# Kernel optimization log

Hardware: AMD Instinct MI355X
Metric: run time of the kernel (lower is better)

Reference implementation:

```python
import jax, jax.numpy as jnp
import numpy as np

B, S, D, H = 8, 1024, 1024, 16
HD = D // H  # head dim = 64


def setup_inputs() -> dict:
    key = jax.random.key(0)
    ks = jax.random.split(key, 8)
    return {
        "hidden_states": jax.random.normal(ks[0], (B, S, D), dtype=jnp.float32),
        "attention_mask": jnp.zeros((B, 1, 1, S), dtype=jnp.float32),
        "Wq": jax.random.normal(ks[1], (D, D), dtype=jnp.float32) * (1.0 / np.sqrt(D)),
        "bq": jax.random.normal(ks[2], (D,), dtype=jnp.float32) * 0.02,
        "Wk": jax.random.normal(ks[3], (D, D), dtype=jnp.float32) * (1.0 / np.sqrt(D)),
        "bk": jax.random.normal(ks[4], (D,), dtype=jnp.float32) * 0.02,
        "Wv": jax.random.normal(ks[5], (D, D), dtype=jnp.float32) * (1.0 / np.sqrt(D)),
        "bv": jax.random.normal(ks[6], (D,), dtype=jnp.float32) * 0.02,
    }


def _split_heads(x):
    # [B,S,D] -> [B,H,S,HD]
    return x.reshape(B, S, H, HD).transpose(0, 2, 1, 3)


def reference(hidden_states, attention_mask, Wq, bq, Wk, bk, Wv, bv):
    q = _split_heads(hidden_states @ Wq + bq)
    k = _split_heads(hidden_states @ Wk + bk)
    v = _split_heads(hidden_states @ Wv + bv)
    # [B,H,S,S]
    scores = jnp.einsum("bhqd,bhkd->bhqk", q, k) / jnp.sqrt(jnp.float32(HD))
    scores = scores + attention_mask
    probs = jax.nn.softmax(scores, axis=-1)  # dropout p=0.0 (eval)
    ctx = jnp.einsum("bhqk,bhkd->bhqd", probs, v)
    # [B,H,S,HD] -> [B,S,D]
    return ctx.transpose(0, 2, 1, 3).reshape(B, S, D)
```

## Files before the change

kernel.cpp:

```cpp
#include <hip/hip_runtime.h>
#include <stdint.h>

#define BB 8
#define SS 1024
#define DD 1024
#define HH 16
#define HDIM 64

typedef __bf16 bf16x8 __attribute__((ext_vector_type(8)));
typedef float f32x4 __attribute__((ext_vector_type(4)));

__device__ __forceinline__ unsigned short f2bf(float f) {
    union { float f; unsigned u; } v; v.f = f;
    unsigned r = v.u + 0x7fff + ((v.u >> 16) & 1);
    return (unsigned short)(r >> 16);
}

__device__ __forceinline__ float exp2fast(float x) {
#if __has_builtin(__builtin_amdgcn_exp2f)
    return __builtin_amdgcn_exp2f(x);
#else
    return __expf(x * 0.69314718f);
#endif
}

__device__ __forceinline__ void async16(void* lds, const void* g) {
    __builtin_amdgcn_global_load_lds(
        (const __attribute__((address_space(1))) unsigned int*)g,
        (__attribute__((address_space(3))) unsigned int*)lds, 16, 0, 0);
}

__global__ __launch_bounds__(256) void convert_x(const float* __restrict__ x,
                                                 unsigned short* __restrict__ xb, int n) {
    int i = (blockIdx.x * 256 + threadIdx.x) * 4;
    if (i < n) {
        float4 f = *reinterpret_cast<const float4*>(x + i);
        ushort4 o;
        o.x = f2bf(f.x); o.y = f2bf(f.y); o.z = f2bf(f.z); o.w = f2bf(f.w);
        *reinterpret_cast<ushort4*>(xb + i) = o;
    }
}

__global__ __launch_bounds__(256) void transpose_w(const float* __restrict__ w0,
                                                   const float* __restrict__ w1,
                                                   const float* __restrict__ w2,
                                                   unsigned short* __restrict__ t0,
                                                   unsigned short* __restrict__ t1,
                                                   unsigned short* __restrict__ t2) {
    const float* w = (blockIdx.z == 0) ? w0 : (blockIdx.z == 1) ? w1 : w2;
    unsigned short* wt = (blockIdx.z == 0) ? t0 : (blockIdx.z == 1) ? t1 : t2;
    __shared__ unsigned short tile[64][65];
    int k0 = blockIdx.x * 64, n0 = blockIdx.y * 64;
    #pragma unroll
    for (int i = 0; i < 16; ++i) {
        int idx = threadIdx.x + i * 256;
        int r = idx >> 6, c = idx & 63;
        tile[r][c] = f2bf(w[(k0 + r) * DD + n0 + c]);
    }
    __syncthreads();
    #pragma unroll
    for (int i = 0; i < 16; ++i) {
        int idx = threadIdx.x + i * 256;
        int r = idx >> 6, c = idx & 63;
        wt[(n0 + r) * DD + k0 + c] = tile[c][r];
    }
}

__global__ __launch_bounds__(256) void gemm_qkv(
    const unsigned short* __restrict__ xb,
    const unsigned short* __restrict__ wt0, const unsigned short* __restrict__ wt1,
    const unsigned short* __restrict__ wt2,
    const float* __restrict__ b0, const float* __restrict__ b1, const float* __restrict__ b2,
    unsigned short* __restrict__ qo, unsigned short* __restrict__ ko,
    unsigned short* __restrict__ vto)
{
    const unsigned short* wt; const float* bias; unsigned short* out;
    if (blockIdx.z == 0)      { wt = wt0; bias = b0; out = qo; }
    else if (blockIdx.z == 1) { wt = wt1; bias = b1; out = ko; }
    else                      { wt = wt2; bias = b2; out = vto; }

    __shared__ unsigned short As[2][128 * 32];
    __shared__ unsigned short Bs[2][128 * 32];

    int m0 = blockIdx.x * 128, n0 = blockIdx.y * 128;
    int tid = threadIdx.x;
    int wave = tid >> 6, lane = tid & 63, lq = lane >> 4, lm = lane & 15;
    int wr = wave >> 1, wc = wave & 1;

    f32x4 acc[4][4] = {};

    int row0 = tid >> 2, s = tid & 3;
    int c0 = (s - (row0 >> 1)) & 3;
    const unsigned short* ga0 = xb + (m0 + row0) * DD + c0 * 8;
    const unsigned short* ga1 = ga0 + 64 * DD;
    const unsigned short* gb0 = wt + (n0 + row0) * DD + c0 * 8;
    const unsigned short* gb1 = gb0 + 64 * DD;

    int slot = ((lq + (lm >> 1)) & 3) * 8;

    async16(&As[0][tid * 8], ga0);  async16(&As[0][(tid + 256) * 8], ga1);
    async16(&Bs[0][tid * 8], gb0);  async16(&Bs[0][(tid + 256) * 8], gb1);
    ga0 += 32; ga1 += 32; gb0 += 32; gb1 += 32;

    for (int t = 0; t < 32; ++t) {
        int p = t & 1;
        __syncthreads();
        if (t < 31) {
            async16(&As[p ^ 1][tid * 8], ga0);  async16(&As[p ^ 1][(tid + 256) * 8], ga1);
            async16(&Bs[p ^ 1][tid * 8], gb0);  async16(&Bs[p ^ 1][(tid + 256) * 8], gb1);
            ga0 += 32; ga1 += 32; gb0 += 32; gb1 += 32;
        }
        bf16x8 a[4], b[4];
        #pragma unroll
        for (int i = 0; i < 4; ++i)
            a[i] = *reinterpret_cast<const bf16x8*>(&As[p][(wr * 64 + i * 16 + lm) * 32 + slot]);
        #pragma unroll
        for (int j = 0; j < 4; ++j)
            b[j] = *reinterpret_cast<const bf16x8*>(&Bs[p][(wc * 64 + j * 16 + lm) * 32 + slot]);
        #pragma unroll
        for (int i = 0; i < 4; ++i)
            #pragma unroll
            for (int j = 0; j < 4; ++j)
                acc[i][j] = __builtin_amdgcn_mfma_f32_16x16x32_bf16(a[i], b[j], acc[i][j], 0, 0, 0);
    }

    if (blockIdx.z == 2) {
        #pragma unroll
        for (int j = 0; j < 4; ++j) {
            int col = n0 + wc * 64 + j * 16 + lm;
            float bsv = bias[col];
            int h = col >> 6, hd = col & 63;
            #pragma unroll
            for (int i = 0; i < 4; ++i) {
                int m = m0 + wr * 64 + i * 16 + lq * 4;
                int b_ = m >> 10, sr = m & 1023;
                ushort4 pk;
                pk.x = f2bf(acc[i][j][0] + bsv);
                pk.y = f2bf(acc[i][j][1] + bsv);
                pk.z = f2bf(acc[i][j][2] + bsv);
                pk.w = f2bf(acc[i][j][3] + bsv);
                *reinterpret_cast<ushort4*>(out + (((b_ * HH + h) * HDIM + hd) << 10) + sr) = pk;
            }
        }
    } else {
        #pragma unroll
        for (int j = 0; j < 4; ++j) {
            int col = n0 + wc * 64 + j * 16 + lm;
            float bsv = bias[col];
            int h = col >> 6, hd = col & 63;
            #pragma unroll
            for (int i = 0; i < 4; ++i) {
                #pragma unroll
                for (int r = 0; r < 4; ++r) {
                    int m = m0 + wr * 64 + i * 16 + lq * 4 + r;
                    int b_ = m >> 10, sr = m & 1023;
                    out[(((b_ * HH + h) << 10) + sr) * HDIM + hd] = f2bf(acc[i][j][r] + bsv);
                }
            }
        }
    }
}

__global__ __launch_bounds__(256) void attention(
    const unsigned short* __restrict__ q,
    const unsigned short* __restrict__ k,
    const unsigned short* __restrict__ vt,
    const float* __restrict__ mask,
    float* __restrict__ out)
{
    __shared__ unsigned short Ks[2][64 * 64];
    __shared__ unsigned short Vs[2][64 * 64];
    __shared__ unsigned short Ps[4][16 * 72];
    __shared__ float msk[SS];

    int blk = blockIdx.x;
    int xcd = blk & 7, j = blk >> 3;
    int bh = (xcd << 4) + (j >> 4);
    int qt = j & 15;
    int b = bh >> 4, h = bh & 15;

    int tid = threadIdx.x;
    int wave = tid >> 6, lane = tid & 63, lq = lane >> 4, lm = lane & 15;

    const unsigned short* qp = q + (size_t)bh * SS * HDIM;
    const unsigned short* kp = k + (size_t)bh * SS * HDIM;
    const unsigned short* vp = vt + (size_t)bh * HDIM * SS;

    for (int i = tid; i < SS; i += 256) msk[i] = mask[b * SS + i] * 1.44269504f;

    int qrow = qt * 64 + wave * 16 + lm;
    bf16x8 qa0 = *reinterpret_cast<const bf16x8*>(qp + qrow * HDIM + lq * 8);
    bf16x8 qa1 = *reinterpret_cast<const bf16x8*>(qp + qrow * HDIM + 32 + lq * 8);

    float lsum = 0.f;
    f32x4 o[4] = {};

    int row0 = tid >> 3, sg = tid & 7;
    int cg = (sg - row0) & 7;
    const unsigned short* gk = kp + row0 * 64 + cg * 8;
    const unsigned short* gv = vp + row0 * SS + cg * 8;

    int sl0 = ((lq + lm) & 7) * 8;
    int sl1 = ((lq + lm + 4) & 7) * 8;

    async16(&Ks[0][tid * 8], gk);  async16(&Ks[0][(tid + 256) * 8], gk + 32 * 64);
    async16(&Vs[0][tid * 8], gv);  async16(&Vs[0][(tid + 256) * 8], gv + 32 * SS);
    gk += 64 * 64; gv += 64;

    unsigned short* Pw = Ps[wave];

    for (int t = 0; t < 16; ++t) {
        int p = t & 1;
        __syncthreads();
        if (t < 15) {
            async16(&Ks[p ^ 1][tid * 8], gk);  async16(&Ks[p ^ 1][(tid + 256) * 8], gk + 32 * 64);
            async16(&Vs[p ^ 1][tid * 8], gv);  async16(&Vs[p ^ 1][(tid + 256) * 8], gv + 32 * SS);
            gk += 64 * 64; gv += 64;
        }
        int kb0 = t * 64;

        f32x4 c[4];
        #pragma unroll
        for (int nb = 0; nb < 4; ++nb) {
            bf16x8 kf0 = *reinterpret_cast<const bf16x8*>(&Ks[p][(nb * 16 + lm) * 64 + sl0]);
            bf16x8 kf1 = *reinterpret_cast<const bf16x8*>(&Ks[p][(nb * 16 + lm) * 64 + sl1]);
            f32x4 z = {};
            z = __builtin_amdgcn_mfma_f32_16x16x32_bf16(kf0, qa0, z, 0, 0, 0);
            z = __builtin_amdgcn_mfma_f32_16x16x32_bf16(kf1, qa1, z, 0, 0, 0);
            c[nb] = z;
        }

        #pragma unroll
        for (int nb = 0; nb < 4; ++nb) {
            float4 mk = *reinterpret_cast<const float4*>(&msk[kb0 + nb * 16 + lq * 4]);
            unsigned u[4];
            #pragma unroll
            for (int r = 0; r < 4; ++r) {
                float e = exp2fast(fmaf(c[nb][r], 0.18033688f,
                                        reinterpret_cast<const float*>(&mk)[r]));
                union { float f; unsigned v; } cv; cv.f = e;
                u[r] = cv.v;
                union { unsigned v; float f; } tr; tr.v = cv.v & 0xffff0000u;
                lsum += tr.f;
            }
            uint2 pk;
            pk.x = __builtin_amdgcn_perm(u[1], u[0], 0x07060302u);
            pk.y = __builtin_amdgcn_perm(u[3], u[2], 0x07060302u);
            *reinterpret_cast<uint2*>(&Pw[lm * 72 + nb * 16 + lq * 4]) = pk;
        }

        #pragma unroll
        for (int ks = 0; ks < 2; ++ks) {
            bf16x8 pa = *reinterpret_cast<const bf16x8*>(&Pw[lm * 72 + ks * 32 + lq * 8]);
            int slv = (ks == 0) ? sl0 : sl1;
            #pragma unroll
            for (int nb2 = 0; nb2 < 4; ++nb2) {
                bf16x8 vf = *reinterpret_cast<const bf16x8*>(&Vs[p][(nb2 * 16 + lm) * 64 + slv]);
                o[nb2] = __builtin_amdgcn_mfma_f32_16x16x32_bf16(pa, vf, o[nb2], 0, 0, 0);
            }
        }
    }

    lsum += __shfl_xor(lsum, 16, 64);
    lsum += __shfl_xor(lsum, 32, 64);
    float linv[4];
    #pragma unroll
    for (int r = 0; r < 4; ++r)
        linv[r] = 1.0f / __shfl(lsum, lq * 4 + r, 64);

    #pragma unroll
    for (int nb2 = 0; nb2 < 4; ++nb2) {
        #pragma unroll
        for (int r = 0; r < 4; ++r) {
            int sr = qt * 64 + wave * 16 + lq * 4 + r;
            out[((size_t)(b * SS + sr)) * DD + h * HDIM + nb2 * 16 + lm] = o[nb2][r] * linv[r];
        }
    }
}

extern "C" void kernel_launch(void* const* d_in, const int* in_sizes, int n_in,
                              void* d_out, int out_size, void* d_ws, size_t ws_size,
                              hipStream_t stream) {
    const float* hs   = (const float*)d_in[0];
    const float* mask = (const float*)d_in[1];
    const float* Wq   = (const float*)d_in[2];
    const float* bq   = (const float*)d_in[3];
    const float* Wk   = (const float*)d_in[4];
    const float* bk   = (const float*)d_in[5];
    const float* Wv   = (const float*)d_in[6];
    const float* bv   = (const float*)d_in[7];
    float* out = (float*)d_out;

    char* ws = (char*)d_ws;
    unsigned short* Xb  = (unsigned short*)(ws);
    unsigned short* WT0 = (unsigned short*)(ws + 16777216);
    unsigned short* WT1 = (unsigned short*)(ws + 18874368);
    unsigned short* WT2 = (unsigned short*)(ws + 20971520);
    unsigned short* qw  = (unsigned short*)(ws + 23068672);
    unsigned short* kw  = (unsigned short*)(ws + 39845888);
    unsigned short* vtw = (unsigned short*)(ws + 56623104);

    convert_x<<<8192, 256, 0, stream>>>(hs, Xb, BB * SS * DD);
    transpose_w<<<dim3(16, 16, 3), 256, 0, stream>>>(Wq, Wk, Wv, WT0, WT1, WT2);
    gemm_qkv<<<dim3(64, 8, 3), 256, 0, stream>>>(Xb, WT0, WT1, WT2,
                                                 bq, bk, bv, qw, kw, vtw);
    attention<<<2048, 256, 0, stream>>>(qw, kw, vtw, mask, out);
}
```

Before: 249.3 us.

## Pre-pack QKV operands into MFMA fragment layout and load directly from global

Merges the x conversion and weight transpose into one prep kernel that writes bf16 data already arranged in MFMA fragment order. The QKV GEMM then reads fragments straight from global memory into registers with software double-buffering, dropping the LDS staging and the barriers that went with it. It also adds XCD-aware block remapping for L2 reuse and stages Q/K output through LDS so stores are coalesced. The bf16 rounding in the epilogue becomes a cheaper round-half-up with a perm instruction. The risk is lower reuse, because every wave now fetches its own operands from L2 instead of sharing one LDS tile across the block.

```diff
diff --git a/kernel.cpp b/kernel.cpp
--- a/kernel.cpp
+++ b/kernel.cpp
@@ -30,133 +30,177 @@
         (__attribute__((address_space(3))) unsigned int*)lds, 16, 0, 0);
 }
 
-__global__ __launch_bounds__(256) void convert_x(const float* __restrict__ x,
-                                                 unsigned short* __restrict__ xb, int n) {
-    int i = (blockIdx.x * 256 + threadIdx.x) * 4;
-    if (i < n) {
-        float4 f = *reinterpret_cast<const float4*>(x + i);
+__global__ __launch_bounds__(256) void prep(
+    const float* __restrict__ x, unsigned short* __restrict__ xf,
+    const float* __restrict__ w0, const float* __restrict__ w1,
+    const float* __restrict__ w2,
+    unsigned short* __restrict__ f0, unsigned short* __restrict__ f1,
+    unsigned short* __restrict__ f2)
+{
+    __shared__ unsigned short tile[64 * 76];
+    int bid = blockIdx.x;
+    int tid = threadIdx.x;
+    if (bid < 2048) {
+        int mt = bid >> 4, kt = bid & 15;
+        const float* src = x + (size_t)(mt * 64) * DD + kt * 64;
+        #pragma unroll
+        for (int i = 0; i < 4; ++i) {
+            int f = tid + i * 256;
+            int r = f >> 4, c4 = f & 15;
+            float4 v = *reinterpret_cast<const float4*>(src + r * DD + c4 * 4);
+            ushort4 o;
+            o.x = f2bf(v.x); o.y = f2bf(v.y); o.z = f2bf(v.z); o.w = f2bf(v.w);
+            *reinterpret_cast<ushort4*>(&tile[r * 76 + c4 * 4]) = o;
+        }
+        __syncthreads();
+        #pragma unroll
+        for (int i = 0; i < 2; ++i) {
+            int s = tid + i * 256;
+            int frag = s >> 6, l = s & 63;
+            int m_l = (frag & 3) * 16 + (l & 15);
+            int k_l = (frag >> 2) * 32 + ((l >> 4) & 3) * 8;
+            uint4 v = *reinterpret_cast<const uint4*>(&tile[m_l * 76 + k_l]);
+            int fm = mt * 4 + (frag & 3);
+            int fk = kt * 2 + (frag >> 2);
+            *reinterpret_cast<uint4*>(xf + (size_t)((fm * 32 + fk) * 64 + l) * 8) = v;
+        }
+        return;
+    }
+    int idx = bid - 2048;
+    int z = idx >> 8, rem = idx & 255;
+    const float* w = (z == 0) ? w0 : (z == 1) ? w1 : w2;
+    unsigned short* wf = (z == 0) ? f0 : (z == 1) ? f1 : f2;
+    int kt = rem & 15, nt = rem >> 4;
+    const float* src = w + (size_t)(kt * 64) * DD + nt * 64;
+    #pragma unroll
+    for (int i = 0; i < 4; ++i) {
+        int f = tid + i * 256;
+        int r = f >> 4, c4 = f & 15;
+        float4 v = *reinterpret_cast<const float4*>(src + r * DD + c4 * 4);
         ushort4 o;
-        o.x = f2bf(f.x); o.y = f2bf(f.y); o.z = f2bf(f.z); o.w = f2bf(f.w);
-        *reinterpret_cast<ushort4*>(xb + i) = o;
-    }
-}
-
-__global__ __launch_bounds__(256) void transpose_w(const float* __restrict__ w0,
-                                                   const float* __restrict__ w1,
-                                                   const float* __restrict__ w2,
-                                                   unsigned short* __restrict__ t0,
-                                                   unsigned short* __restrict__ t1,
-                                                   unsigned short* __restrict__ t2) {
-    const float* w = (blockIdx.z == 0) ? w0 : (blockIdx.z == 1) ? w1 : w2;
-    unsigned short* wt = (blockIdx.z == 0) ? t0 : (blockIdx.z == 1) ? t1 : t2;
-    __shared__ unsigned short tile[64][65];
-    int k0 = blockIdx.x * 64, n0 = blockIdx.y * 64;
-    #pragma unroll
-    for (int i = 0; i < 16; ++i) {
-        int idx = threadIdx.x + i * 256;
-        int r = idx >> 6, c = idx & 63;
-        tile[r][c] = f2bf(w[(k0 + r) * DD + n0 + c]);
+        o.x = f2bf(v.x); o.y = f2bf(v.y); o.z = f2bf(v.z); o.w = f2bf(v.w);
+        *reinterpret_cast<ushort4*>(&tile[r * 76 + c4 * 4]) = o;
     }
     __syncthreads();
     #pragma unroll
-    for (int i = 0; i < 16; ++i) {
-        int idx = threadIdx.x + i * 256;
-        int r = idx >> 6, c = idx & 63;
-        wt[(n0 + r) * DD + k0 + c] = tile[c][r];
-    }
-}
-
-__global__ __launch_bounds__(256) void gemm_qkv(
-    const unsigned short* __restrict__ xb,
-    const unsigned short* __restrict__ wt0, const unsigned short* __restrict__ wt1,
-    const unsigned short* __restrict__ wt2,
+    for (int i = 0; i < 2; ++i) {
+        int s = tid + i * 256;
+        int frag = s >> 6, l = s & 63;
+        int n_l = (frag & 3) * 16 + (l & 15);
+        int k_l = (frag >> 2) * 32 + ((l >> 4) & 3) * 8;
+        unsigned short tmp[8];
+        #pragma unroll
+        for (int j = 0; j < 8; ++j) tmp[j] = tile[(k_l + j) * 76 + n_l];
+        int fn = nt * 4 + (frag & 3);
+        int fk = kt * 2 + (frag >> 2);
+        *reinterpret_cast<uint4*>(wf + (size_t)((fn * 32 + fk) * 64 + l) * 8) =
+            *reinterpret_cast<const uint4*>(tmp);
+    }
+}
+
+__global__ __launch_bounds__(256, 3) void gemm_qkv(
+    const unsigned short* __restrict__ xf,
+    const unsigned short* __restrict__ wf0, const unsigned short* __restrict__ wf1,
+    const unsigned short* __restrict__ wf2,
     const float* __restrict__ b0, const float* __restrict__ b1, const float* __restrict__ b2,
     unsigned short* __restrict__ qo, unsigned short* __restrict__ ko,
     unsigned short* __restrict__ vto)
 {
-    const unsigned short* wt; const float* bias; unsigned short* out;
-    if (blockIdx.z == 0)      { wt = wt0; bias = b0; out = qo; }
-    else if (blockIdx.z == 1) { wt = wt1; bias = b1; out = ko; }
-    else                      { wt = wt2; bias = b2; out = vto; }
-
-    __shared__ unsigned short As[2][128 * 32];
-    __shared__ unsigned short Bs[2][128 * 32];
-
-    int m0 = blockIdx.x * 128, n0 = blockIdx.y * 128;
+    int bid = blockIdx.x;
+    int xcd = bid & 7, g = bid >> 3;
+    int strip = xcd * 3 + (g % 3);
+    int mt = g / 3;
+    int nt = strip & 7, z = strip >> 3;
+
+    const unsigned short* wf; const float* bias; unsigned short* out;
+    if (z == 0)      { wf = wf0; bias = b0; out = qo; }
+    else if (z == 1) { wf = wf1; bias = b1; out = ko; }
+    else             { wf = wf2; bias = b2; out = vto; }
+
+    __shared__ unsigned short stg[4][64 * 76];
+
     int tid = threadIdx.x;
     int wave = tid >> 6, lane = tid & 63, lq = lane >> 4, lm = lane & 15;
     int wr = wave >> 1, wc = wave & 1;
 
+    const unsigned short* aB = xf + (size_t)((mt * 8 + wr * 4) * 32) * 512 + lane * 8;
+    const unsigned short* bB = wf + (size_t)((nt * 8 + wc * 4) * 32) * 512 + lane * 8;
+
     f32x4 acc[4][4] = {};
-
-    int row0 = tid >> 2, s = tid & 3;
-    int c0 = (s - (row0 >> 1)) & 3;
-    const unsigned short* ga0 = xb + (m0 + row0) * DD + c0 * 8;
-    const unsigned short* ga1 = ga0 + 64 * DD;
-    const unsigned short* gb0 = wt + (n0 + row0) * DD + c0 * 8;
-    const unsigned short* gb1 = gb0 + 64 * DD;
-
-    int slot = ((lq + (lm >> 1)) & 3) * 8;
-
-    async16(&As[0][tid * 8], ga0);  async16(&As[0][(tid + 256) * 8], ga1);
-    async16(&Bs[0][tid * 8], gb0);  async16(&Bs[0][(tid + 256) * 8], gb1);
-    ga0 += 32; ga1 += 32; gb0 += 32; gb1 += 32;
-
-    for (int t = 0; t < 32; ++t) {
-        int p = t & 1;
-        __syncthreads();
-        if (t < 31) {
-            async16(&As[p ^ 1][tid * 8], ga0);  async16(&As[p ^ 1][(tid + 256) * 8], ga1);
-            async16(&Bs[p ^ 1][tid * 8], gb0);  async16(&Bs[p ^ 1][(tid + 256) * 8], gb1);
-            ga0 += 32; ga1 += 32; gb0 += 32; gb1 += 32;
-        }
-        bf16x8 a[4], b[4];
-        #pragma unroll
-        for (int i = 0; i < 4; ++i)
-            a[i] = *reinterpret_cast<const bf16x8*>(&As[p][(wr * 64 + i * 16 + lm) * 32 + slot]);
-        #pragma unroll
-        for (int j = 0; j < 4; ++j)
-            b[j] = *reinterpret_cast<const bf16x8*>(&Bs[p][(wc * 64 + j * 16 + lm) * 32 + slot]);
-        #pragma unroll
-        for (int i = 0; i < 4; ++i)
-            #pragma unroll
-            for (int j = 0; j < 4; ++j)
-                acc[i][j] = __builtin_amdgcn_mfma_f32_16x16x32_bf16(a[i], b[j], acc[i][j], 0, 0, 0);
-    }
-
-    if (blockIdx.z == 2) {
+    bf16x8 a0[4], a1[4], bb0[4], bb1[4];
+
+#define LDFRAGS(AB, BB, T)                                                     \
+    {                                                                          \
+        _Pragma("unroll") for (int i_ = 0; i_ < 4; ++i_)                       \
+            AB[i_] = *reinterpret_cast<const bf16x8*>(aB + (i_ * 32 + (T)) * 512); \
+        _Pragma("unroll") for (int j_ = 0; j_ < 4; ++j_)                       \
+            BB[j_] = *reinterpret_cast<const bf16x8*>(bB + (j_ * 32 + (T)) * 512); \
+    }
+#define MFMAS(AB, BB)                                                          \
+    {                                                                          \
+        _Pragma("unroll") for (int i_ = 0; i_ < 4; ++i_)                       \
+            _Pragma("unroll") for (int j_ = 0; j_ < 4; ++j_)                   \
+                acc[i_][j_] = __builtin_amdgcn_mfma_f32_16x16x32_bf16(         \
+                    AB[i_], BB[j_], acc[i_][j_], 0, 0, 0);                     \
+    }
+
+    LDFRAGS(a0, bb0, 0);
+    for (int tt = 0; tt < 16; ++tt) {
+        int t = tt * 2;
+        LDFRAGS(a1, bb1, t + 1);
+        MFMAS(a0, bb0);
+        LDFRAGS(a0, bb0, t + 2);
+        MFMAS(a1, bb1);
+    }
+#undef LDFRAGS
+#undef MFMAS
+
+    int m0 = mt * 128;
+    int col0 = nt * 128 + wc * 64;
+    if (z == 2) {
         #pragma unroll
         for (int j = 0; j < 4; ++j) {
-            int col = n0 + wc * 64 + j * 16 + lm;
+            int col = col0 + j * 16 + lm;
             float bsv = bias[col];
             int h = col >> 6, hd = col & 63;
             #pragma unroll
             for (int i = 0; i < 4; ++i) {
                 int m = m0 + wr * 64 + i * 16 + lq * 4;
                 int b_ = m >> 10, sr = m & 1023;
-                ushort4 pk;
-                pk.x = f2bf(acc[i][j][0] + bsv);
-                pk.y = f2bf(acc[i][j][1] + bsv);
-                pk.z = f2bf(acc[i][j][2] + bsv);
-                pk.w = f2bf(acc[i][j][3] + bsv);
-                *reinterpret_cast<ushort4*>(out + (((b_ * HH + h) * HDIM + hd) << 10) + sr) = pk;
+                union { float f; unsigned u; } p0, p1, p2, p3;
+                p0.f = acc[i][j][0] + bsv; p1.f = acc[i][j][1] + bsv;
+                p2.f = acc[i][j][2] + bsv; p3.f = acc[i][j][3] + bsv;
+                uint2 pk;
+                pk.x = __builtin_amdgcn_perm(p1.u + 0x8000u, p0.u + 0x8000u, 0x07060302u);
+                pk.y = __builtin_amdgcn_perm(p3.u + 0x8000u, p2.u + 0x8000u, 0x07060302u);
+                *reinterpret_cast<uint2*>(out + (((b_ * HH + h) * HDIM + hd) << 10) + sr) = pk;
             }
         }
     } else {
+        unsigned short* S = stg[wave];
         #pragma unroll
         for (int j = 0; j < 4; ++j) {
-            int col = n0 + wc * 64 + j * 16 + lm;
-            float bsv = bias[col];
-            int h = col >> 6, hd = col & 63;
+            float bsv = bias[col0 + j * 16 + lm];
             #pragma unroll
             for (int i = 0; i < 4; ++i) {
                 #pragma unroll
                 for (int r = 0; r < 4; ++r) {
-                    int m = m0 + wr * 64 + i * 16 + lq * 4 + r;
-                    int b_ = m >> 10, sr = m & 1023;
-                    out[(((b_ * HH + h) << 10) + sr) * HDIM + hd] = f2bf(acc[i][j][r] + bsv);
+                    union { float f; unsigned u; } cv; cv.f = acc[i][j][r] + bsv;
+                    S[(i * 16 + lq * 4 + r) * 76 + j * 16 + lm] =
+                        (unsigned short)((cv.u + 0x8000u) >> 16);
                 }
             }
+        }
+        int h = col0 >> 6;
+        int mrow = m0 + wr * 64;
+        int b_ = mrow >> 10, sr0 = mrow & 1023;
+        unsigned short* ob = out + ((size_t)((b_ * HH + h) << 10) + sr0) * HDIM;
+        #pragma unroll
+        for (int u = 0; u < 8; ++u) {
+            int s = lane + u * 64;
+            int row = s >> 3, c8 = s & 7;
+            uint4 v = *reinterpret_cast<const uint4*>(&S[row * 76 + c8 * 8]);
+            *reinterpret_cast<uint4*>(ob + row * HDIM + c8 * 8) = v;
         }
     }
 }
@@ -292,17 +336,16 @@
     float* out = (float*)d_out;
 
     char* ws = (char*)d_ws;
-    unsigned short* Xb  = (unsigned short*)(ws);
-    unsigned short* WT0 = (unsigned short*)(ws + 16777216);
-    unsigned short* WT1 = (unsigned short*)(ws + 18874368);
-    unsigned short* WT2 = (unsigned short*)(ws + 20971520);
+    unsigned short* XF  = (unsigned short*)(ws);
+    unsigned short* WF0 = (unsigned short*)(ws + 16777216);
+    unsigned short* WF1 = (unsigned short*)(ws + 18874368);
+    unsigned short* WF2 = (unsigned short*)(ws + 20971520);
     unsigned short* qw  = (unsigned short*)(ws + 23068672);
     unsigned short* kw  = (unsigned short*)(ws + 39845888);
     unsigned short* vtw = (unsigned short*)(ws + 56623104);
 
-    convert_x<<<8192, 256, 0, stream>>>(hs, Xb, BB * SS * DD);
-    transpose_w<<<dim3(16, 16, 3), 256, 0, stream>>>(Wq, Wk, Wv, WT0, WT1, WT2);
-    gemm_qkv<<<dim3(64, 8, 3), 256, 0, stream>>>(Xb, WT0, WT1, WT2,
-                                                 bq, bk, bv, qw, kw, vtw);
+    prep<<<2816, 256, 0, stream>>>(hs, XF, Wq, Wk, Wv, WF0, WF1, WF2);
+    gemm_qkv<<<1536, 256, 0, stream>>>(XF, WF0, WF1, WF2,
+                                       bq, bk, bv, qw, kw, vtw);
     attention<<<2048, 256, 0, stream>>>(qw, kw, vtw, mask, out);
 }
```

New measurement: 232.6 us. 6.7% less time.
